# Kernel optimization log

Measured on AMD Instinct MI355X. Metric: run time of the kernel, lower is better.

The kernel has to match this reference:

```python
import jax, jax.numpy as jnp
import numpy as np

NEG_SLOPE = 0.2

def gat_layer(x, src, dst, W, b, a_src, a_dst, heads, out_dim, concat):
    N = x.shape[0]
    h = (x @ W).reshape(N, heads, out_dim)            # [N,H,D]
    s_src = jnp.sum(h * a_src, axis=-1)               # [N,H]
    s_dst = jnp.sum(h * a_dst, axis=-1)               # [N,H]
    e = jax.nn.leaky_relu(s_src[src] + s_dst[dst], NEG_SLOPE)  # [E,H]
    # segment softmax over destination nodes (self-loops guarantee nonempty segments)
    m = jax.ops.segment_max(e, dst, num_segments=N)
    e = jnp.exp(e - m[dst])
    denom = jax.ops.segment_sum(e, dst, num_segments=N)
    alpha = e / denom[dst]                            # [E,H]
    msg = h[src] * alpha[:, :, None]                  # [E,H,D]
    out = jax.ops.segment_sum(msg, dst, num_segments=N)  # [N,H,D]
    if concat:
        out = out.reshape(N, heads * out_dim)
    else:
        out = out.mean(axis=1)
    return out + b

def setup_inputs() -> dict:
    key = jax.random.key(0)
    ks = jax.random.split(key, 16)
    N, E = 50000, 1600000
    IN, HID, OUT, H = 128, 256, 32, 4
    D = HID // H
    def glorot(k, shape):
        fan = shape[0] + shape[-1]
        return jax.random.uniform(k, shape, jnp.float32, -1.0, 1.0) * np.sqrt(6.0 / fan)
    x = jax.random.normal(ks[0], (N, IN), jnp.float32)
    edge_index = jax.random.randint(ks[1], (2, E), 0, N, jnp.int32)
    return {
        "x": x, "edge_index": edge_index,
        "W0": glorot(ks[2], (IN, H * D)), "b0": jnp.zeros((H * D,), jnp.float32),
        "asrc0": glorot(ks[3], (H, D)), "adst0": glorot(ks[4], (H, D)),
        "W1": glorot(ks[5], (HID, H * D)), "b1": jnp.zeros((H * D,), jnp.float32),
        "asrc1": glorot(ks[6], (H, D)), "adst1": glorot(ks[7], (H, D)),
        "W2": glorot(ks[8], (HID, 1 * OUT)), "b2": jnp.zeros((OUT,), jnp.float32),
        "asrc2": glorot(ks[9], (1, OUT)), "adst2": glorot(ks[10], (1, OUT)),
    }

def reference(x, edge_index, W0, b0, asrc0, adst0, W1, b1, asrc1, adst1, W2, b2, asrc2, adst2):
    N = x.shape[0]
    # add self-loops (PyG GATConv default)
    loop = jnp.arange(N, dtype=edge_index.dtype)
    src = jnp.concatenate([edge_index[0], loop])
    dst = jnp.concatenate([edge_index[1], loop])
    h = gat_layer(x, src, dst, W0, b0, asrc0, adst0, heads=4, out_dim=64, concat=True)
    h = jax.nn.elu(h)
    h = gat_layer(h, src, dst, W1, b1, asrc1, adst1, heads=4, out_dim=64, concat=True)
    h = jax.nn.elu(h)
    h = gat_layer(h, src, dst, W2, b2, asrc2, adst2, heads=1, out_dim=32, concat=False)
    return jax.nn.log_softmax(h, axis=1)
```

## Files before the change

kernel.cpp:

```cpp
#include <hip/hip_runtime.h>
#include <hip/hip_bf16.h>
#include <math.h>

#define IN_DIM 128
#define HID    256
#define OUTD   32
#define HEADS  4
#define NB_SH  7
#define BUCKET_CAP 6144
#define NCHUNK_BLKS 256

typedef __attribute__((ext_vector_type(8))) short s8v;
typedef __attribute__((ext_vector_type(4))) float f4v;

__device__ inline unsigned short f2bf(float f) {
    union { __hip_bfloat16 b; unsigned short u; } cv;
    cv.b = __float2bfloat16(f);
    return cv.u;
}


__global__ __launch_bounds__(256) void csr_hist(const int* __restrict__ ei,
                                                int* __restrict__ H,
                                                int E, int N, int NB, int per_blk) {
    __shared__ int hist[512];
    int t = threadIdx.x;
    for (int i = t; i < NB; i += 256) hist[i] = 0;
    __syncthreads();
    int lo = blockIdx.x * per_blk;
    int hi = min(lo + per_blk, E + N);
    for (int e = lo + t; e < hi; e += 256) {
        int dst = (e < E) ? ei[E + e] : (e - E);
        atomicAdd(&hist[dst >> NB_SH], 1);
    }
    __syncthreads();
    for (int i = t; i < NB; i += 256) H[blockIdx.x * NB + i] = hist[i];
}

__global__ __launch_bounds__(256) void csr_colscan(int* __restrict__ H,
                                                   int* __restrict__ total, int NB) {
    int b = blockIdx.x, t = threadIdx.x;
    int v = H[t * NB + b];
    __shared__ int s[256];
    s[t] = v;
    __syncthreads();
    for (int o = 1; o < 256; o <<= 1) {
        int x = (t >= o) ? s[t - o] : 0;
        __syncthreads();
        s[t] += x;
        __syncthreads();
    }
    H[t * NB + b] = s[t] - v;
    if (t == 255) total[b] = s[255];
}

__global__ void csr_basescan(const int* __restrict__ total, int* __restrict__ base, int NB) {
    __shared__ int s[512];
    int t = threadIdx.x;
    int v = (t < NB) ? total[t] : 0;
    s[t] = v;
    __syncthreads();
    for (int o = 1; o < 512; o <<= 1) {
        int x = (t >= o) ? s[t - o] : 0;
        __syncthreads();
        s[t] += x;
        __syncthreads();
    }
    if (t < NB) base[t] = s[t] - v;
    if (t == NB - 1) base[NB] = s[t];
}

__global__ __launch_bounds__(256) void csr_partition(const int* __restrict__ ei,
                                                     const int* __restrict__ H,
                                                     const int* __restrict__ base,
                                                     int* __restrict__ ebuf,
                                                     int E, int N, int per_blk, int NB) {
    __shared__ int cur[512];
    int t = threadIdx.x;
    for (int i = t; i < NB; i += 256) cur[i] = base[i] + H[blockIdx.x * NB + i];
    __syncthreads();
    int lo = blockIdx.x * per_blk;
    int hi = min(lo + per_blk, E + N);
    for (int e = lo + t; e < hi; e += 256) {
        int src = (e < E) ? ei[e] : (e - E);
        int dst = (e < E) ? ei[E + e] : (e - E);
        int pos = atomicAdd(&cur[dst >> NB_SH], 1);
        ebuf[pos] = src | ((dst & 127) << 16);
    }
}

__global__ __launch_bounds__(256) void csr_sort(const int* __restrict__ ebuf,
                                                const int* __restrict__ base,
                                                int* __restrict__ col,
                                                int* __restrict__ rp, int N, int NB) {
    int b = blockIdx.x, t = threadIdx.x;
    int lo = base[b], hi = base[b + 1];
    int nbase = b << NB_SH;
    __shared__ int c_[128], sc[128], cur[128];
    __shared__ int loc[BUCKET_CAP];
    if (t < 128) c_[t] = 0;
    __syncthreads();
    for (int k = lo + t; k < hi; k += 256) atomicAdd(&c_[(ebuf[k] >> 16) & 127], 1);
    __syncthreads();
    if (t < 128) sc[t] = c_[t];
    __syncthreads();
    for (int o = 1; o < 128; o <<= 1) {
        int x = 0;
        if (t < 128 && t >= o) x = sc[t - o];
        __syncthreads();
        if (t < 128) sc[t] += x;
        __syncthreads();
    }
    if (t < 128) {
        int excl = sc[t] - c_[t];
        cur[t] = excl;
        int node = nbase + t;
        if (node < N) rp[node] = lo + excl;
    }
    if (b == NB - 1 && t == 0) rp[N] = hi;
    __syncthreads();
    for (int k = lo + t; k < hi; k += 256) {
        int e = ebuf[k];
        int p = atomicAdd(&cur[(e >> 16) & 127], 1);
        if (p < BUCKET_CAP) loc[p] = e & 0xFFFF;
    }
    __syncthreads();
    int m = min(hi - lo, BUCKET_CAP);
    for (int k = t; k < m; k += 256) col[lo + k] = loc[k];
}


__global__ __launch_bounds__(256) void prep_w(const float* __restrict__ W,
                                              unsigned short* __restrict__ Wt_h,
                                              unsigned short* __restrict__ Wt_l,
                                              int K, int N) {
    int idx = blockIdx.x * 256 + threadIdx.x;
    if (idx >= K * N) return;
    int n = idx / K, k = idx % K;
    float x = W[(size_t)k * N + n];
    unsigned short h = f2bf(x);
    float hf = __uint_as_float((unsigned)h << 16);
    Wt_h[idx] = h;
    Wt_l[idx] = f2bf(x - hf);
}


template <int BN>
__global__ __launch_bounds__(256, 2) void gemm_mfma(const float* __restrict__ A,
                                                    const unsigned short* __restrict__ Wt_h,
                                                    const unsigned short* __restrict__ Wt_l,
                                                    float* __restrict__ C,
                                                    unsigned short* __restrict__ Cb,
                                                    int M, int K, int Nst) {
    constexpr int WROWS = (BN == 128) ? 64 : 32;
    constexpr int WCOLS = (BN == 128) ? 64 : 32;
    constexpr int MI = WROWS / 16, NJ = WCOLS / 16;
    __shared__ unsigned short As_h[128][64], As_l[128][64];
    __shared__ unsigned short Bs_h[BN][64], Bs_l[BN][64];
    int tid = threadIdx.x;
    int lane = tid & 63, w = tid >> 6;
    int wm, wn;
    if (BN == 128) { wm = w & 1; wn = w >> 1; } else { wm = w; wn = 0; }
    int row0 = blockIdx.x * 128, col0 = blockIdx.y * BN;

    f4v acc[MI][NJ];
#pragma unroll
    for (int i = 0; i < MI; i++)
#pragma unroll
        for (int j = 0; j < NJ; j++) acc[i][j] = (f4v)(0.f);

    for (int k0 = 0; k0 < K; k0 += 64) {
#pragma unroll
        for (int i = 0; i < 4; i++) {
            int c = tid + i * 256;
            int r = c >> 3, ch = c & 7;
            int grow = row0 + r;
            float x[8];
            if (grow < M) {
                float4 v0 = *(const float4*)(A + (size_t)grow * K + k0 + ch * 8);
                float4 v1 = *(const float4*)(A + (size_t)grow * K + k0 + ch * 8 + 4);
                x[0] = v0.x; x[1] = v0.y; x[2] = v0.z; x[3] = v0.w;
                x[4] = v1.x; x[5] = v1.y; x[6] = v1.z; x[7] = v1.w;
            } else {
#pragma unroll
                for (int j = 0; j < 8; j++) x[j] = 0.f;
            }
            union { unsigned short u[8]; uint4 q; } hu, lu;
#pragma unroll
            for (int j = 0; j < 8; j++) {
                hu.u[j] = f2bf(x[j]);
                float hf = __uint_as_float((unsigned)hu.u[j] << 16);
                lu.u[j] = f2bf(x[j] - hf);
            }
            int chs = ch ^ (r & 7);
            *(uint4*)&As_h[r][chs * 8] = hu.q;
            *(uint4*)&As_l[r][chs * 8] = lu.q;
        }
#pragma unroll
        for (int i = 0; i < BN * 8 / 256; i++) {
            int c = tid + i * 256;
            int n = c >> 3, ch = c & 7;
            int chs = ch ^ (n & 7);
            size_t g = (size_t)(col0 + n) * K + k0 + ch * 8;
            *(uint4*)&Bs_h[n][chs * 8] = *(const uint4*)(Wt_h + g);
            *(uint4*)&Bs_l[n][chs * 8] = *(const uint4*)(Wt_l + g);
        }
        __syncthreads();
#pragma unroll
        for (int ks = 0; ks < 2; ks++) {
            s8v ah[MI], al[MI], bh[NJ], bl[NJ];
            int kc = ks * 4 + (lane >> 4);
            int lr = lane & 15;
#pragma unroll
            for (int i = 0; i < MI; i++) {
                int r = wm * WROWS + i * 16 + lr;
                ah[i] = *(const s8v*)&As_h[r][(kc ^ (r & 7)) * 8];
                al[i] = *(const s8v*)&As_l[r][(kc ^ (r & 7)) * 8];
            }
#pragma unroll
            for (int j = 0; j < NJ; j++) {
                int n = wn * WCOLS + j * 16 + lr;
                bh[j] = *(const s8v*)&Bs_h[n][(kc ^ (n & 7)) * 8];
                bl[j] = *(const s8v*)&Bs_l[n][(kc ^ (n & 7)) * 8];
            }
#pragma unroll
            for (int i = 0; i < MI; i++)
#pragma unroll
                for (int j = 0; j < NJ; j++) {
                    acc[i][j] = __builtin_amdgcn_mfma_f32_16x16x32_bf16(ah[i], bh[j], acc[i][j], 0, 0, 0);
                    acc[i][j] = __builtin_amdgcn_mfma_f32_16x16x32_bf16(ah[i], bl[j], acc[i][j], 0, 0, 0);
                    acc[i][j] = __builtin_amdgcn_mfma_f32_16x16x32_bf16(al[i], bh[j], acc[i][j], 0, 0, 0);
                }
        }
        __syncthreads();
    }
    int lr = lane & 15, lg = lane >> 4;
#pragma unroll
    for (int i = 0; i < MI; i++)
#pragma unroll
        for (int j = 0; j < NJ; j++) {
            int gcol = col0 + wn * WCOLS + j * 16 + lr;
#pragma unroll
            for (int rr = 0; rr < 4; rr++) {
                int grow = row0 + wm * WROWS + i * 16 + lg * 4 + rr;
                if (grow < M) {
                    float v = acc[i][j][rr];
                    C[(size_t)grow * Nst + gcol] = v;
                    Cb[(size_t)grow * Nst + gcol] = f2bf(v);
                }
            }
        }
}


template <int CH, int H>
__global__ __launch_bounds__(256) void compute_scores(const float* __restrict__ h,
                                                      const float* __restrict__ a_src,
                                                      const float* __restrict__ a_dst,
                                                      float* __restrict__ s_src,
                                                      float* __restrict__ s_dst, int N) {
    const int D = CH / H;
    const int NPB = 256 / CH;
    int t = threadIdx.x;
    int n = blockIdx.x * NPB + t / CH;
    if (n >= N) return;
    int c = t % CH;
    float v = h[(size_t)n * CH + c];
    float vs = v * a_src[c];
    float vd = v * a_dst[c];
#pragma unroll
    for (int o = D / 2; o > 0; o >>= 1) {
        vs += __shfl_xor(vs, o, D);
        vd += __shfl_xor(vd, o, D);
    }
    if ((c % D) == 0) {
        int head = c / D;
        s_src[(size_t)n * H + head] = vs;
        s_dst[(size_t)n * H + head] = vd;
    }
}


template <int H>
__global__ __launch_bounds__(256) void edge_softmax(const float* __restrict__ ssrc,
                                                    const float* __restrict__ sdst,
                                                    const int* __restrict__ rp,
                                                    const int* __restrict__ col,
                                                    float* __restrict__ alpha, int N) {
    const int SL = 64 / H;
    int wave = threadIdx.x >> 6;
    int lane = threadIdx.x & 63;
    int n = blockIdx.x * 4 + wave;
    if (n >= N) return;
    int head = lane % H;
    int slot = lane / H;
    int k0 = rp[n], k1 = rp[n + 1];
    float sd = sdst[(size_t)n * H + head];
    float m = -1e30f, l = 0.f;
    for (int k = k0 + slot; k < k1; k += SL) {
        int s = col[k];
        float e = ssrc[(size_t)s * H + head] + sd;
        e = (e > 0.f) ? e : 0.2f * e;
        float mn = fmaxf(m, e);
        l = l * __expf(m - mn) + __expf(e - mn);
        m = mn;
    }
#pragma unroll
    for (int off = H; off < 64; off <<= 1) {
        float m2 = __shfl_xor(m, off, 64);
        float l2 = __shfl_xor(l, off, 64);
        float mn = fmaxf(m, m2);
        l = l * __expf(m - mn) + l2 * __expf(m2 - mn);
        m = mn;
    }
    float inv = 1.f / l;
    for (int k = k0 + slot; k < k1; k += SL) {
        int s = col[k];
        float e = ssrc[(size_t)s * H + head] + sd;
        e = (e > 0.f) ? e : 0.2f * e;
        alpha[(size_t)k * H + head] = __expf(e - m) * inv;
    }
}


template <int CH, int H, int MODE>
__global__ __launch_bounds__(256) void gat_gather(const unsigned short* __restrict__ hb,
                                                  const float* __restrict__ alpha,
                                                  const int* __restrict__ rp,
                                                  const int* __restrict__ col,
                                                  const float* __restrict__ bias,
                                                  float* __restrict__ out, int N) {
    const int TPE = CH / 8;
    const int EPW = 64 / TPE;
    const int D = CH / H;
    int wv = threadIdx.x >> 6, lane = threadIdx.x & 63;
    int n = blockIdx.x * 4 + wv;
    if (n >= N) return;
    int eo = lane / TPE;
    int c = (lane % TPE) * 8;
    int head = c / D;
    int k0 = __builtin_amdgcn_readfirstlane(rp[n]);
    int k1 = __builtin_amdgcn_readfirstlane(rp[n + 1]);
    float acc[8];
#pragma unroll
    for (int j = 0; j < 8; j++) acc[j] = 0.f;
    for (int k = k0; k < k1; k += 2 * EPW) {
        int ka = k + eo, kb = k + EPW + eo;
        bool oa = ka < k1, ob = kb < k1;
        int sa = col[oa ? ka : k0];
        int sb = col[ob ? kb : k0];
        float a0 = oa ? alpha[(size_t)ka * H + head] : 0.f;
        float a1 = ob ? alpha[(size_t)kb * H + head] : 0.f;
        uint4 ha = *(const uint4*)(hb + (size_t)sa * CH + c);
        uint4 hc = *(const uint4*)(hb + (size_t)sb * CH + c);
        const unsigned* pa = (const unsigned*)&ha;
        const unsigned* pb = (const unsigned*)&hc;
#pragma unroll
        for (int q = 0; q < 4; q++) {
            acc[2 * q]     += a0 * __uint_as_float(pa[q] << 16);
            acc[2 * q + 1] += a0 * __uint_as_float(pa[q] & 0xffff0000u);
            acc[2 * q]     += a1 * __uint_as_float(pb[q] << 16);
            acc[2 * q + 1] += a1 * __uint_as_float(pb[q] & 0xffff0000u);
        }
    }
#pragma unroll
    for (int off = TPE; off < 64; off <<= 1)
#pragma unroll
        for (int j = 0; j < 8; j++) acc[j] += __shfl_xor(acc[j], off);
    if (eo != 0) return;
    float o[8];
#pragma unroll
    for (int j = 0; j < 8; j++) o[j] = acc[j] + bias[c + j];
    if (MODE == 0) {
#pragma unroll
        for (int j = 0; j < 8; j++) o[j] = (o[j] > 0.f) ? o[j] : expm1f(o[j]);
    } else {
        float mx = o[0];
#pragma unroll
        for (int j = 1; j < 8; j++) mx = fmaxf(mx, o[j]);
#pragma unroll
        for (int off = 1; off < TPE; off <<= 1) mx = fmaxf(mx, __shfl_xor(mx, off));
        float sm = 0.f;
#pragma unroll
        for (int j = 0; j < 8; j++) sm += __expf(o[j] - mx);
#pragma unroll
        for (int off = 1; off < TPE; off <<= 1) sm += __shfl_xor(sm, off);
        float lg = logf(sm) + mx;
#pragma unroll
        for (int j = 0; j < 8; j++) o[j] -= lg;
    }
    float4* op = (float4*)(out + (size_t)n * CH + c);
    op[0] = make_float4(o[0], o[1], o[2], o[3]);
    op[1] = make_float4(o[4], o[5], o[6], o[7]);
}


extern "C" void kernel_launch(void* const* d_in, const int* in_sizes, int n_in,
                              void* d_out, int out_size, void* d_ws, size_t ws_size,
                              hipStream_t stream) {
    const float* x   = (const float*)d_in[0];
    const int*   ei  = (const int*)d_in[1];
    const float* W0  = (const float*)d_in[2];
    const float* b0  = (const float*)d_in[3];
    const float* as0 = (const float*)d_in[4];
    const float* ad0 = (const float*)d_in[5];
    const float* W1  = (const float*)d_in[6];
    const float* b1  = (const float*)d_in[7];
    const float* as1 = (const float*)d_in[8];
    const float* ad1 = (const float*)d_in[9];
    const float* W2  = (const float*)d_in[10];
    const float* b2  = (const float*)d_in[11];
    const float* as2 = (const float*)d_in[12];
    const float* ad2 = (const float*)d_in[13];

    int N = in_sizes[0] / IN_DIM;
    int E = in_sizes[1] / 2;
    int Et = E + N;
    int NB = (N + 127) >> NB_SH;

    char* w = (char*)d_ws;
    size_t off = 0;
    auto alloc = [&](size_t bytes) -> void* {
        void* p = w + off;
        off = (off + bytes + 255) & ~(size_t)255;
        return p;
    };
    float*          P     = (float*)alloc((size_t)N * HID * 4);
    float*          Q     = (float*)alloc((size_t)N * HID * 4);
    unsigned short* Ab    = (unsigned short*)alloc((size_t)N * HID * 2);
    float*          ssrc  = (float*)alloc((size_t)N * HEADS * 4);
    float*          sdst  = (float*)alloc((size_t)N * HEADS * 4);
    float*          alpha = (float*)alloc((size_t)Et * HEADS * 4);
    int*            rp    = (int*)alloc((size_t)(N + 1) * 4);
    int*            col   = (int*)alloc((size_t)Et * 4);
    int*            H     = (int*)alloc((size_t)NCHUNK_BLKS * NB * 4);
    int*            total = (int*)alloc((size_t)(NB + 1) * 4);
    int*            base  = (int*)alloc((size_t)(NB + 1) * 4);
    int*            ebuf  = (int*)alloc((size_t)Et * 4);
    unsigned short* Wt0h  = (unsigned short*)alloc((size_t)IN_DIM * HID * 2);
    unsigned short* Wt0l  = (unsigned short*)alloc((size_t)IN_DIM * HID * 2);
    unsigned short* Wt1h  = (unsigned short*)alloc((size_t)HID * HID * 2);
    unsigned short* Wt1l  = (unsigned short*)alloc((size_t)HID * HID * 2);
    unsigned short* Wt2h  = (unsigned short*)alloc((size_t)HID * OUTD * 2);
    unsigned short* Wt2l  = (unsigned short*)alloc((size_t)HID * OUTD * 2);

    prep_w<<<(IN_DIM * HID + 255) / 256, 256, 0, stream>>>(W0, Wt0h, Wt0l, IN_DIM, HID);
    prep_w<<<(HID * HID + 255) / 256, 256, 0, stream>>>(W1, Wt1h, Wt1l, HID, HID);
    prep_w<<<(HID * OUTD + 255) / 256, 256, 0, stream>>>(W2, Wt2h, Wt2l, HID, OUTD);

    int per_blk = (Et + NCHUNK_BLKS - 1) / NCHUNK_BLKS;
    csr_hist<<<NCHUNK_BLKS, 256, 0, stream>>>(ei, H, E, N, NB, per_blk);
    csr_colscan<<<NB, 256, 0, stream>>>(H, total, NB);
    csr_basescan<<<1, 512, 0, stream>>>(total, base, NB);
    csr_partition<<<NCHUNK_BLKS, 256, 0, stream>>>(ei, H, base, ebuf, E, N, per_blk, NB);
    csr_sort<<<NB, 256, 0, stream>>>(ebuf, base, col, rp, N, NB);

    dim3 gm((N + 127) / 128, 2);
    dim3 gm2((N + 127) / 128, 1);

    gemm_mfma<128><<<gm, 256, 0, stream>>>(x, Wt0h, Wt0l, P, Ab, N, IN_DIM, HID);
    compute_scores<HID, HEADS><<<N, 256, 0, stream>>>(P, as0, ad0, ssrc, sdst, N);
    edge_softmax<HEADS><<<(N + 3) / 4, 256, 0, stream>>>(ssrc, sdst, rp, col, alpha, N);
    gat_gather<HID, HEADS, 0><<<(N + 3) / 4, 256, 0, stream>>>(Ab, alpha, rp, col, b0, Q, N);

    gemm_mfma<128><<<gm, 256, 0, stream>>>(Q, Wt1h, Wt1l, P, Ab, N, HID, HID);
    compute_scores<HID, HEADS><<<N, 256, 0, stream>>>(P, as1, ad1, ssrc, sdst, N);
    edge_softmax<HEADS><<<(N + 3) / 4, 256, 0, stream>>>(ssrc, sdst, rp, col, alpha, N);
    gat_gather<HID, HEADS, 0><<<(N + 3) / 4, 256, 0, stream>>>(Ab, alpha, rp, col, b1, Q, N);

    gemm_mfma<32><<<gm2, 256, 0, stream>>>(Q, Wt2h, Wt2l, P, Ab, N, HID, OUTD);
    compute_scores<OUTD, 1><<<(N + 7) / 8, 256, 0, stream>>>(P, as2, ad2, ssrc, sdst, N);
    edge_softmax<1><<<(N + 3) / 4, 256, 0, stream>>>(ssrc, sdst, rp, col, alpha, N);
    gat_gather<OUTD, 1, 1><<<(N + 3) / 4, 256, 0, stream>>>(Ab, alpha, rp, col, b2,
                                                            (float*)d_out, N);
}
```

Measured before the change: 521.2 us.

## Fuse attention scores into GEMM epilogue and softmax into gather

The GEMM epilogue now computes the per-head source and destination attention scores straight from the accumulators using a 16-lane shuffle reduction, so the fp32 feature matrix is no longer stored and the separate score kernel is gone. The edge softmax is merged into the gather kernel. Each wave first computes the per-node max and sum, then recomputes each edge's exponent inline while aggregating. This drops the alpha array write and read and two launches per layer. The gather loop is also unrolled to four edge groups for more memory-level parallelism, at the cost of recomputing the exponent per channel lane and extra ssrc gathers.

New measurement: 422.1 us. -19.0%, faster.

```diff
diff --git a/kernel.cpp b/kernel.cpp
--- a/kernel.cpp
+++ b/kernel.cpp
@@ -149,9 +149,12 @@
 __global__ __launch_bounds__(256, 2) void gemm_mfma(const float* __restrict__ A,
                                                     const unsigned short* __restrict__ Wt_h,
                                                     const unsigned short* __restrict__ Wt_l,
-                                                    float* __restrict__ C,
                                                     unsigned short* __restrict__ Cb,
-                                                    int M, int K, int Nst) {
+                                                    const float* __restrict__ asrc,
+                                                    const float* __restrict__ adst,
+                                                    float* __restrict__ ssrcO,
+                                                    float* __restrict__ sdstO,
+                                                    int M, int K, int Nst, int Hn) {
     constexpr int WROWS = (BN == 128) ? 64 : 32;
     constexpr int WCOLS = (BN == 128) ? 64 : 32;
     constexpr int MI = WROWS / 16, NJ = WCOLS / 16;
@@ -243,124 +246,118 @@
 #pragma unroll
             for (int rr = 0; rr < 4; rr++) {
                 int grow = row0 + wm * WROWS + i * 16 + lg * 4 + rr;
-                if (grow < M) {
-                    float v = acc[i][j][rr];
-                    C[(size_t)grow * Nst + gcol] = v;
-                    Cb[(size_t)grow * Nst + gcol] = f2bf(v);
-                }
-            }
-        }
-}
-
-
-template <int CH, int H>
-__global__ __launch_bounds__(256) void compute_scores(const float* __restrict__ h,
-                                                      const float* __restrict__ a_src,
-                                                      const float* __restrict__ a_dst,
-                                                      float* __restrict__ s_src,
-                                                      float* __restrict__ s_dst, int N) {
-    const int D = CH / H;
-    const int NPB = 256 / CH;
-    int t = threadIdx.x;
-    int n = blockIdx.x * NPB + t / CH;
-    if (n >= N) return;
-    int c = t % CH;
-    float v = h[(size_t)n * CH + c];
-    float vs = v * a_src[c];
-    float vd = v * a_dst[c];
-#pragma unroll
-    for (int o = D / 2; o > 0; o >>= 1) {
-        vs += __shfl_xor(vs, o, D);
-        vd += __shfl_xor(vd, o, D);
-    }
-    if ((c % D) == 0) {
-        int head = c / D;
-        s_src[(size_t)n * H + head] = vs;
-        s_dst[(size_t)n * H + head] = vd;
-    }
-}
-
-
-template <int H>
-__global__ __launch_bounds__(256) void edge_softmax(const float* __restrict__ ssrc,
-                                                    const float* __restrict__ sdst,
-                                                    const int* __restrict__ rp,
-                                                    const int* __restrict__ col,
-                                                    float* __restrict__ alpha, int N) {
-    const int SL = 64 / H;
-    int wave = threadIdx.x >> 6;
-    int lane = threadIdx.x & 63;
-    int n = blockIdx.x * 4 + wave;
-    if (n >= N) return;
-    int head = lane % H;
-    int slot = lane / H;
-    int k0 = rp[n], k1 = rp[n + 1];
-    float sd = sdst[(size_t)n * H + head];
-    float m = -1e30f, l = 0.f;
-    for (int k = k0 + slot; k < k1; k += SL) {
-        int s = col[k];
-        float e = ssrc[(size_t)s * H + head] + sd;
-        e = (e > 0.f) ? e : 0.2f * e;
-        float mn = fmaxf(m, e);
-        l = l * __expf(m - mn) + __expf(e - mn);
-        m = mn;
-    }
-#pragma unroll
-    for (int off = H; off < 64; off <<= 1) {
-        float m2 = __shfl_xor(m, off, 64);
-        float l2 = __shfl_xor(l, off, 64);
-        float mn = fmaxf(m, m2);
-        l = l * __expf(m - mn) + l2 * __expf(m2 - mn);
-        m = mn;
-    }
-    float inv = 1.f / l;
-    for (int k = k0 + slot; k < k1; k += SL) {
-        int s = col[k];
-        float e = ssrc[(size_t)s * H + head] + sd;
-        e = (e > 0.f) ? e : 0.2f * e;
-        alpha[(size_t)k * H + head] = __expf(e - m) * inv;
-    }
+                if (grow < M) Cb[(size_t)grow * Nst + gcol] = f2bf(acc[i][j][rr]);
+            }
+        }
+    int hd = (BN == 128) ? (blockIdx.y * 2 + wn) : 0;
+    float as_[NJ], ad_[NJ];
+#pragma unroll
+    for (int j = 0; j < NJ; j++) {
+        int gcol = col0 + wn * WCOLS + j * 16 + lr;
+        as_[j] = asrc[gcol];
+        ad_[j] = adst[gcol];
+    }
+#pragma unroll
+    for (int i = 0; i < MI; i++)
+#pragma unroll
+        for (int rr = 0; rr < 4; rr++) {
+            float ps = 0.f, pd = 0.f;
+#pragma unroll
+            for (int j = 0; j < NJ; j++) {
+                ps += acc[i][j][rr] * as_[j];
+                pd += acc[i][j][rr] * ad_[j];
+            }
+#pragma unroll
+            for (int off = 1; off < 16; off <<= 1) {
+                ps += __shfl_xor(ps, off);
+                pd += __shfl_xor(pd, off);
+            }
+            int grow = row0 + wm * WROWS + i * 16 + lg * 4 + rr;
+            if (lr == 0 && grow < M) {
+                ssrcO[(size_t)grow * Hn + hd] = ps;
+                sdstO[(size_t)grow * Hn + hd] = pd;
+            }
+        }
 }
 
 
 template <int CH, int H, int MODE>
-__global__ __launch_bounds__(256) void gat_gather(const unsigned short* __restrict__ hb,
-                                                  const float* __restrict__ alpha,
-                                                  const int* __restrict__ rp,
-                                                  const int* __restrict__ col,
-                                                  const float* __restrict__ bias,
-                                                  float* __restrict__ out, int N) {
+__global__ __launch_bounds__(256) void gat_fused(const unsigned short* __restrict__ hb,
+                                                 const float* __restrict__ ssrc,
+                                                 const float* __restrict__ sdst,
+                                                 const int* __restrict__ rp,
+                                                 const int* __restrict__ col,
+                                                 const float* __restrict__ bias,
+                                                 float* __restrict__ out, int N) {
     const int TPE = CH / 8;
     const int EPW = 64 / TPE;
     const int D = CH / H;
     int wv = threadIdx.x >> 6, lane = threadIdx.x & 63;
     int n = blockIdx.x * 4 + wv;
     if (n >= N) return;
+    int k0 = __builtin_amdgcn_readfirstlane(rp[n]);
+    int k1 = __builtin_amdgcn_readfirstlane(rp[n + 1]);
+
+    int h1 = lane % H;
+    int slot = lane / H;
+    const int SL = 64 / H;
+    float sd1 = sdst[(size_t)n * H + h1];
+    float m = -1e30f, l = 0.f;
+    for (int k = k0 + slot; k < k1; k += SL) {
+        int s = col[k];
+        float e = ssrc[(size_t)s * H + h1] + sd1;
+        e = (e > 0.f) ? e : 0.2f * e;
+        float mn = fmaxf(m, e);
+        l = l * __expf(m - mn) + __expf(e - mn);
+        m = mn;
+    }
+#pragma unroll
+    for (int off = H; off < 64; off <<= 1) {
+        float m2 = __shfl_xor(m, off);
+        float l2 = __shfl_xor(l, off);
+        float mn = fmaxf(m, m2);
+        l = l * __expf(m - mn) + l2 * __expf(m2 - mn);
+        m = mn;
+    }
+
     int eo = lane / TPE;
     int c = (lane % TPE) * 8;
     int head = c / D;
-    int k0 = __builtin_amdgcn_readfirstlane(rp[n]);
-    int k1 = __builtin_amdgcn_readfirstlane(rp[n + 1]);
+    float mh = __shfl(m, head);
+    float invl = 1.f / __shfl(l, head);
+    float sdh = __shfl(sd1, head);
+
     float acc[8];
 #pragma unroll
     for (int j = 0; j < 8; j++) acc[j] = 0.f;
-    for (int k = k0; k < k1; k += 2 * EPW) {
-        int ka = k + eo, kb = k + EPW + eo;
-        bool oa = ka < k1, ob = kb < k1;
-        int sa = col[oa ? ka : k0];
-        int sb = col[ob ? kb : k0];
-        float a0 = oa ? alpha[(size_t)ka * H + head] : 0.f;
-        float a1 = ob ? alpha[(size_t)kb * H + head] : 0.f;
-        uint4 ha = *(const uint4*)(hb + (size_t)sa * CH + c);
-        uint4 hc = *(const uint4*)(hb + (size_t)sb * CH + c);
-        const unsigned* pa = (const unsigned*)&ha;
-        const unsigned* pb = (const unsigned*)&hc;
-#pragma unroll
-        for (int q = 0; q < 4; q++) {
-            acc[2 * q]     += a0 * __uint_as_float(pa[q] << 16);
-            acc[2 * q + 1] += a0 * __uint_as_float(pa[q] & 0xffff0000u);
-            acc[2 * q]     += a1 * __uint_as_float(pb[q] << 16);
-            acc[2 * q + 1] += a1 * __uint_as_float(pb[q] & 0xffff0000u);
+
+    for (int k = k0; k < k1; k += 4 * EPW) {
+        int ss[4];
+        float aa[4];
+#pragma unroll
+        for (int u = 0; u < 4; u++) {
+            int ku = k + u * EPW + eo;
+            bool v = ku < k1;
+            ss[u] = col[v ? ku : k0];
+            aa[u] = v ? invl : 0.f;
+        }
+#pragma unroll
+        for (int u = 0; u < 4; u++) {
+            float e = ssrc[(size_t)ss[u] * H + head] + sdh;
+            e = (e > 0.f) ? e : 0.2f * e;
+            aa[u] *= __expf(e - mh);
+        }
+        uint4 hv[4];
+#pragma unroll
+        for (int u = 0; u < 4; u++) hv[u] = *(const uint4*)(hb + (size_t)ss[u] * CH + c);
+#pragma unroll
+        for (int u = 0; u < 4; u++) {
+            const unsigned* p = (const unsigned*)&hv[u];
+#pragma unroll
+            for (int q = 0; q < 4; q++) {
+                acc[2 * q]     += aa[u] * __uint_as_float(p[q] << 16);
+                acc[2 * q + 1] += aa[u] * __uint_as_float(p[q] & 0xffff0000u);
+            }
         }
     }
 #pragma unroll
@@ -425,12 +422,10 @@
         off = (off + bytes + 255) & ~(size_t)255;
         return p;
     };
-    float*          P     = (float*)alloc((size_t)N * HID * 4);
     float*          Q     = (float*)alloc((size_t)N * HID * 4);
     unsigned short* Ab    = (unsigned short*)alloc((size_t)N * HID * 2);
     float*          ssrc  = (float*)alloc((size_t)N * HEADS * 4);
     float*          sdst  = (float*)alloc((size_t)N * HEADS * 4);
-    float*          alpha = (float*)alloc((size_t)Et * HEADS * 4);
     int*            rp    = (int*)alloc((size_t)(N + 1) * 4);
     int*            col   = (int*)alloc((size_t)Et * 4);
     int*            H     = (int*)alloc((size_t)NCHUNK_BLKS * NB * 4);
@@ -457,20 +452,18 @@
 
     dim3 gm((N + 127) / 128, 2);
     dim3 gm2((N + 127) / 128, 1);
-
-    gemm_mfma<128><<<gm, 256, 0, stream>>>(x, Wt0h, Wt0l, P, Ab, N, IN_DIM, HID);
-    compute_scores<HID, HEADS><<<N, 256, 0, stream>>>(P, as0, ad0, ssrc, sdst, N);
-    edge_softmax<HEADS><<<(N + 3) / 4, 256, 0, stream>>>(ssrc, sdst, rp, col, alpha, N);
-    gat_gather<HID, HEADS, 0><<<(N + 3) / 4, 256, 0, stream>>>(Ab, alpha, rp, col, b0, Q, N);
-
-    gemm_mfma<128><<<gm, 256, 0, stream>>>(Q, Wt1h, Wt1l, P, Ab, N, HID, HID);
-    compute_scores<HID, HEADS><<<N, 256, 0, stream>>>(P, as1, ad1, ssrc, sdst, N);
-    edge_softmax<HEADS><<<(N + 3) / 4, 256, 0, stream>>>(ssrc, sdst, rp, col, alpha, N);
-    gat_gather<HID, HEADS, 0><<<(N + 3) / 4, 256, 0, stream>>>(Ab, alpha, rp, col, b1, Q, N);
-
-    gemm_mfma<32><<<gm2, 256, 0, stream>>>(Q, Wt2h, Wt2l, P, Ab, N, HID, OUTD);
-    compute_scores<OUTD, 1><<<(N + 7) / 8, 256, 0, stream>>>(P, as2, ad2, ssrc, sdst, N);
-    edge_softmax<1><<<(N + 3) / 4, 256, 0, stream>>>(ssrc, sdst, rp, col, alpha, N);
-    gat_gather<OUTD, 1, 1><<<(N + 3) / 4, 256, 0, stream>>>(Ab, alpha, rp, col, b2,
-                                                            (float*)d_out, N);
-}
+    int gg = (N + 3) / 4;
+
+    gemm_mfma<128><<<gm, 256, 0, stream>>>(x, Wt0h, Wt0l, Ab, as0, ad0, ssrc, sdst,
+                                           N, IN_DIM, HID, HEADS);
+    gat_fused<HID, HEADS, 0><<<gg, 256, 0, stream>>>(Ab, ssrc, sdst, rp, col, b0, Q, N);
+
+    gemm_mfma<128><<<gm, 256, 0, stream>>>(Q, Wt1h, Wt1l, Ab, as1, ad1, ssrc, sdst,
+                                           N, HID, HID, HEADS);
+    gat_fused<HID, HEADS, 0><<<gg, 256, 0, stream>>>(Ab, ssrc, sdst, rp, col, b1, Q, N);
+
+    gemm_mfma<32><<<gm2, 256, 0, stream>>>(Q, Wt2h, Wt2l, Ab, as2, ad2, ssrc, sdst,
+                                           N, HID, OUTD, 1);
+    gat_fused<OUTD, 1, 1><<<gg, 256, 0, stream>>>(Ab, ssrc, sdst, rp, col, b2,
+                                                  (float*)d_out, N);
+}
```
